# Performance work log

Measured on AMD Instinct MI355X. Metric: run time of the kernel, lower is better.

## Reference

```python
import jax, jax.numpy as jnp
import numpy as np

B, S, D, H, DFF, N_LAYERS, BLK = 4, 1024, 1024, 16, 4096, 4, 64
DH = D // H
LN_EPS = 1e-5


def setup_inputs() -> dict:
    key = jax.random.key(0)
    ks = jax.random.split(key, 13)
    s = 0.02
    L = N_LAYERS
    return {
        "x": jax.random.normal(ks[0], (B, S, D), jnp.float32),
        "in_proj_w": jax.random.normal(ks[1], (L, 3 * D, D), jnp.float32) * s,
        "in_proj_b": jnp.zeros((L, 3 * D), jnp.float32),
        "out_w": jax.random.normal(ks[2], (L, D, D), jnp.float32) * s,
        "out_b": jnp.zeros((L, D), jnp.float32),
        "ln1_w": jnp.ones((L, D), jnp.float32),
        "ln1_b": jnp.zeros((L, D), jnp.float32),
        "lin1_w": jax.random.normal(ks[3], (L, DFF, D), jnp.float32) * s,
        "lin1_b": jnp.zeros((L, DFF), jnp.float32),
        "lin2_w": jax.random.normal(ks[4], (L, D, DFF), jnp.float32) * s,
        "lin2_b": jnp.zeros((L, D), jnp.float32),
        "ln2_w": jnp.ones((L, D), jnp.float32),
        "ln2_b": jnp.zeros((L, D), jnp.float32),
    }


def _layer_norm(x, w, b):
    mu = jnp.mean(x, axis=-1, keepdims=True)
    var = jnp.mean(jnp.square(x - mu), axis=-1, keepdims=True)
    return (x - mu) * jax.lax.rsqrt(var + LN_EPS) * w + b


def _forward(x, in_proj_w, in_proj_b, out_w, out_b, ln1_w, ln1_b,
             lin1_w, lin1_b, lin2_w, lin2_b, ln2_w, ln2_b):
    # block-causal additive bias: token may attend to current and previous blocks
    blk = jnp.arange(S) // BLK
    bias = jnp.where(blk[:, None] >= blk[None, :], 0.0, -jnp.inf)  # [S,S]
    scale = 1.0 / np.sqrt(DH).astype(np.float32)

    for l in range(N_LAYERS):
        # --- self-attention (post-norm, PyTorch TransformerEncoderLayer default) ---
        qkv = x @ in_proj_w[l].T + in_proj_b[l]            # [B,S,3D]
        q, k, v = jnp.split(qkv, 3, axis=-1)
        q = q.reshape(B, S, H, DH).transpose(0, 2, 1, 3)   # [B,H,S,DH]
        k = k.reshape(B, S, H, DH).transpose(0, 2, 1, 3)
        v = v.reshape(B, S, H, DH).transpose(0, 2, 1, 3)
        scores = jnp.einsum('bhqd,bhkd->bhqk', q, k) * scale + bias
        attn = jax.nn.softmax(scores, axis=-1)
        o = jnp.einsum('bhqk,bhkd->bhqd', attn, v)
        o = o.transpose(0, 2, 1, 3).reshape(B, S, D)
        o = o @ out_w[l].T + out_b[l]
        x = _layer_norm(x + o, ln1_w[l], ln1_b[l])
        # --- feed-forward (relu) ---
        h = jax.nn.relu(x @ lin1_w[l].T + lin1_b[l]) @ lin2_w[l].T + lin2_b[l]
        x = _layer_norm(x + h, ln2_w[l], ln2_b[l])
    return x


def reference(x, in_proj_w, in_proj_b, out_w, out_b, ln1_w, ln1_b,
              lin1_w, lin1_b, lin2_w, lin2_b, ln2_w, ln2_b):
    return _forward(x, in_proj_w, in_proj_b, out_w, out_b, ln1_w, ln1_b,
                    lin1_w, lin1_b, lin2_w, lin2_b, ln2_w, ln2_b)
```

## Files before the change

### kernel.cpp

```cpp
#include <hip/hip_runtime.h>
#include <stdint.h>

typedef __bf16 bf16;
typedef __bf16 bf16x8 __attribute__((ext_vector_type(8)));
typedef __bf16 bf16x4 __attribute__((ext_vector_type(4)));
typedef float  f32x4  __attribute__((ext_vector_type(4)));

#define B_   4
#define S_   1024
#define D_   1024
#define H_   16
#define DH_  64
#define DFF_ 4096
#define NL_  4
#define M_   (B_*S_)

__device__ __forceinline__ void async_copy16(const void* g, void* l) {
  __builtin_amdgcn_global_load_lds(
      (const __attribute__((address_space(1))) char*)(uintptr_t)g,
      (__attribute__((address_space(3))) char*)(uintptr_t)l,
      16, 0, 0);
}

#define WAITV4 asm volatile("s_waitcnt vmcnt(4)" ::: "memory")
#define WAITV0 asm volatile("s_waitcnt vmcnt(0)" ::: "memory")
#define BAR()  { asm volatile("" ::: "memory"); __builtin_amdgcn_s_barrier(); \
                 asm volatile("" ::: "memory"); }

template<int RELU, int MODE, int QKV, int PH>
__global__ __launch_bounds__(512, 2) void gemm256_kernel(
    const bf16* __restrict__ A,
    const bf16* __restrict__ W,
    const float* __restrict__ bias,
    bf16*  __restrict__ Cb,
    bf16*  __restrict__ VtOut,
    int N, int Ktot, int Kc, int gx, int PN, int PM, int bpk)
{
  __shared__ __align__(16) bf16 As[2][2][256*32];
  __shared__ __align__(16) bf16 Bs[2][2][256*32];

  const int tid  = threadIdx.x;
  const int wave = tid >> 6;
  const int lane = tid & 63;
  const int wr = wave >> 2, wc = wave & 3;
  const int q4  = lane >> 4;
  const int l15 = lane & 15;

  const int Lg  = blockIdx.x;
  const int kz  = Lg / bpk;
  const int L   = Lg % bpk;
  const int xcd = L & 7;
  const int s   = L >> 3;
  const int Gn  = gx / PN;
  const int bn = ((xcd % Gn)*PN + (s % PN)) << 8;
  const int bm = ((xcd / Gn)*PM + (s / PN)) << 8;
  const int kstart = kz * Kc;

  const int r_loc = lane >> 2, c4 = lane & 3;
  const int sko = (c4 ^ ((r_loc >> 1) & 3)) << 3;
  const bf16* agp[2]; const bf16* wgp[2];
#pragma unroll
  for (int j = 0; j < 2; ++j) {
    const int rr = j*128 + wave*16 + r_loc;
    agp[j] = A + (size_t)(bm + rr)*Ktot + kstart + sko;
    wgp[j] = W + (size_t)(bn + rr)*Ktot + kstart + sko;
  }

  auto stageA = [&](int buf, int kk, int koff) {
#pragma unroll
    for (int j = 0; j < 2; ++j)
      async_copy16(agp[j] + koff + kk*32, &As[buf][kk][(j*128 + wave*16)*32]);
  };
  auto stageB = [&](int buf, int kk, int koff) {
#pragma unroll
    for (int j = 0; j < 2; ++j)
      async_copy16(wgp[j] + koff + kk*32, &Bs[buf][kk][(j*128 + wave*16)*32]);
  };

  const int ch = ((q4 ^ ((l15 >> 1) & 3)) << 3);

  f32x4 acc[8][4] = {};
  const int steps = Kc / 64;

  stageA(0, 0, 0); stageB(0, 0, 0); stageA(0, 1, 0); stageB(0, 1, 0);
  WAITV4;
  BAR();

  int koff = 64;
  for (int t = 0; t < steps; ++t) {
    const int c = t & 1;
    const bool pf = (t + 1 < steps);
    if constexpr (PH == 4) {
      bf16x8 bfr[4];
#pragma unroll
      for (int p = 0; p < 4; ++p) {
        const int kk = p >> 1, rh = p & 1;
        if (rh == 0) {
#pragma unroll
          for (int cf = 0; cf < 4; ++cf)
            bfr[cf] = *(const bf16x8*)&Bs[c][kk][(wc*64 + cf*16 + l15)*32 + ch];
        }
        bf16x8 af[4];
#pragma unroll
        for (int r4 = 0; r4 < 4; ++r4)
          af[r4] = *(const bf16x8*)&As[c][kk][(wr*128 + (rh*4 + r4)*16 + l15)*32 + ch];
        if (pf) {
          if      (p == 0) stageA(c ^ 1, 0, koff);
          else if (p == 1) stageB(c ^ 1, 0, koff);
          else if (p == 2) stageA(c ^ 1, 1, koff);
          else             stageB(c ^ 1, 1, koff);
        }
        BAR();
        __builtin_amdgcn_s_setprio(1);
#pragma unroll
        for (int r4 = 0; r4 < 4; ++r4)
#pragma unroll
          for (int cf = 0; cf < 4; ++cf)
            acc[rh*4 + r4][cf] = __builtin_amdgcn_mfma_f32_16x16x32_bf16(
                af[r4], bfr[cf], acc[rh*4 + r4][cf], 0, 0, 0);
        __builtin_amdgcn_s_setprio(0);
        if (p == 1) { if (pf) { WAITV4; } else { WAITV0; } }
        if (p == 3) { if (pf) { WAITV4; } }
        BAR();
      }
    } else {
#pragma unroll
      for (int kk = 0; kk < 2; ++kk) {
        if (pf) { stageA(c ^ 1, kk, koff); stageB(c ^ 1, kk, koff); }
        bf16x8 bfr[4];
#pragma unroll
        for (int cf = 0; cf < 4; ++cf)
          bfr[cf] = *(const bf16x8*)&Bs[c][kk][(wc*64 + cf*16 + l15)*32 + ch];
        bf16x8 af[8];
#pragma unroll
        for (int r = 0; r < 8; ++r)
          af[r] = *(const bf16x8*)&As[c][kk][(wr*128 + r*16 + l15)*32 + ch];
        BAR();
        __builtin_amdgcn_s_setprio(1);
#pragma unroll
        for (int r = 0; r < 8; ++r)
#pragma unroll
          for (int cf = 0; cf < 4; ++cf)
            acc[r][cf] = __builtin_amdgcn_mfma_f32_16x16x32_bf16(
                af[r], bfr[cf], acc[r][cf], 0, 0, 0);
        __builtin_amdgcn_s_setprio(0);
        if (kk == 0) { if (pf) { WAITV4; } else { WAITV0; } }
        else         { if (pf) { WAITV4; } }
        BAR();
      }
    }
    koff += 64;
  }

  if (QKV && bn >= 2*D_) {
#pragma unroll
    for (int r = 0; r < 8; ++r) {
      const int row0 = bm + wr*128 + r*16 + q4*4;
      const int bidx = row0 >> 10, s0 = row0 & 1023;
#pragma unroll
      for (int cf = 0; cf < 4; ++cf) {
        const int col  = bn + wc*64 + cf*16 + l15;
        const int dcol = col - 2*D_;
        const int hh = dcol >> 6, dd = dcol & 63;
        const float bv = bias[col];
        bf16x4 pk;
#pragma unroll
        for (int i = 0; i < 4; ++i) pk[i] = (bf16)(acc[r][cf][i] + bv);
        *(bf16x4*)&VtOut[((size_t)((bidx*H_ + hh)*64 + dd))*S_ + s0] = pk;
      }
    }
  } else if (MODE == 2) {
    bf16* Cpz = Cb + (size_t)kz * ((size_t)M_ * N);
#pragma unroll
    for (int r = 0; r < 8; ++r) {
      const int row0 = bm + wr*128 + r*16 + q4*4;
#pragma unroll
      for (int cf = 0; cf < 4; ++cf) {
        const int col = bn + wc*64 + cf*16 + l15;
#pragma unroll
        for (int i = 0; i < 4; ++i)
          Cpz[(size_t)(row0 + i)*N + col] = (bf16)acc[r][cf][i];
      }
    }
  } else {
#pragma unroll
    for (int r = 0; r < 8; ++r) {
      const int row0 = bm + wr*128 + r*16 + q4*4;
#pragma unroll
      for (int cf = 0; cf < 4; ++cf) {
        const int col = bn + wc*64 + cf*16 + l15;
        const float bv = bias[col];
#pragma unroll
        for (int i = 0; i < 4; ++i) {
          float v = acc[r][cf][i] + bv;
          if (RELU) v = fmaxf(v, 0.f);
          Cb[(size_t)(row0 + i)*N + col] = (bf16)v;
        }
      }
    }
  }
}

template<int RELU, int MODE, int BK>
__global__ __launch_bounds__(256) void gemm_bt_kernel(
    const bf16* __restrict__ A, const bf16* __restrict__ W,
    const float* __restrict__ bias, bf16* __restrict__ Cb,
    int N, int Ktot, int Kc, int gx, int PN, int PM, int bpk)
{
  constexpr int NI = (BK == 64) ? 4 : 2;
  __shared__ bf16 As[2][128*BK];
  __shared__ bf16 Bs[2][128*BK];

  const int tid  = threadIdx.x;
  const int wave = tid >> 6;
  const int lane = tid & 63;
  const int wr = wave >> 1, wc = wave & 1;
  const int q4  = lane >> 4;
  const int l15 = lane & 15;

  const int Lg  = blockIdx.x;
  const int kz  = Lg / bpk;
  const int L   = Lg % bpk;
  const int xcd = L & 7;
  const int s   = L >> 3;
  const int Gn  = gx / PN;
  const int bn = ((xcd % Gn)*PN + (s % PN)) << 7;
  const int bm = ((xcd / Gn)*PM + (s / PN)) << 7;
  const int kstart = kz * Kc;

  const bf16* agp[NI]; const bf16* wgp[NI];
  int ldsb[NI];
  if constexpr (BK == 64) {
    const int r_loc = lane >> 3, c8 = lane & 7;
#pragma unroll
    for (int j = 0; j < NI; ++j) {
      const int rr = wave*32 + j*8 + r_loc;
      const int ko = ((c8 ^ (rr & 7)) << 3);
      agp[j] = A + (size_t)(bm + rr)*Ktot + kstart + ko;
      wgp[j] = W + (size_t)(bn + rr)*Ktot + kstart + ko;
      ldsb[j] = (wave*32 + j*8) * 64;
    }
  } else {
    const int r_loc = lane >> 2, c4 = lane & 3;
#pragma unroll
    for (int j = 0; j < NI; ++j) {
      const int rr = wave*32 + j*16 + r_loc;
      const int ko = ((c4 ^ ((rr >> 1) & 3)) << 3);
      agp[j] = A + (size_t)(bm + rr)*Ktot + kstart + ko;
      wgp[j] = W + (size_t)(bn + rr)*Ktot + kstart + ko;
      ldsb[j] = (wave*32 + j*16) * 32;
    }
  }

  f32x4 acc[4][4] = {};
  const int steps = Kc / BK;

  auto stage = [&](int buf) {
#pragma unroll
    for (int j = 0; j < NI; ++j) {
      async_copy16(agp[j], &As[buf][ldsb[j]]);
      async_copy16(wgp[j], &Bs[buf][ldsb[j]]);
      agp[j] += BK; wgp[j] += BK;
    }
  };

  const int sl32 = (l15 >> 1) & 3;
  const int sl64 = l15 & 7;

  auto compute = [&](int buf) {
    if constexpr (BK == 64) {
#pragma unroll
      for (int kk = 0; kk < 2; ++kk) {
        const int ch = (((kk << 2) | q4) ^ sl64) << 3;
        bf16x8 af[4], bfr[4];
#pragma unroll
        for (int rf = 0; rf < 4; ++rf)
          af[rf] = *(const bf16x8*)&As[buf][(wr*64 + rf*16 + l15)*64 + ch];
#pragma unroll
        for (int cf = 0; cf < 4; ++cf)
          bfr[cf] = *(const bf16x8*)&Bs[buf][(wc*64 + cf*16 + l15)*64 + ch];
#pragma unroll
        for (int rf = 0; rf < 4; ++rf)
#pragma unroll
          for (int cf = 0; cf < 4; ++cf)
            acc[rf][cf] = __builtin_amdgcn_mfma_f32_16x16x32_bf16(
                af[rf], bfr[cf], acc[rf][cf], 0, 0, 0);
      }
    } else {
      const int ch = (q4 ^ sl32) << 3;
      bf16x8 af[4], bfr[4];
#pragma unroll
      for (int rf = 0; rf < 4; ++rf)
        af[rf] = *(const bf16x8*)&As[buf][(wr*64 + rf*16 + l15)*32 + ch];
#pragma unroll
      for (int cf = 0; cf < 4; ++cf)
        bfr[cf] = *(const bf16x8*)&Bs[buf][(wc*64 + cf*16 + l15)*32 + ch];
#pragma unroll
      for (int rf = 0; rf < 4; ++rf)
#pragma unroll
        for (int cf = 0; cf < 4; ++cf)
          acc[rf][cf] = __builtin_amdgcn_mfma_f32_16x16x32_bf16(
              af[rf], bfr[cf], acc[rf][cf], 0, 0, 0);
    }
  };

  stage(0);
  __syncthreads();
  for (int k = 0; k < steps; ++k) {
    const int cur = k & 1;
    if (k + 1 < steps) stage(cur ^ 1);
    compute(cur);
    __syncthreads();
  }

  if (MODE == 2) {
    bf16* Cpz = Cb + (size_t)kz * ((size_t)M_ * N);
#pragma unroll
    for (int r = 0; r < 4; ++r) {
      const int row0 = bm + wr*64 + r*16 + q4*4;
#pragma unroll
      for (int c = 0; c < 4; ++c) {
        const int col = bn + wc*64 + c*16 + l15;
#pragma unroll
        for (int i = 0; i < 4; ++i)
          Cpz[(size_t)(row0 + i)*N + col] = (bf16)acc[r][c][i];
      }
    }
  } else {
#pragma unroll
    for (int r = 0; r < 4; ++r) {
      const int row0 = bm + wr*64 + r*16 + q4*4;
#pragma unroll
      for (int c = 0; c < 4; ++c) {
        const int col = bn + wc*64 + c*16 + l15;
        const float bv = bias[col];
#pragma unroll
        for (int i = 0; i < 4; ++i) {
          float v = acc[r][c][i] + bv;
          if (RELU) v = fmaxf(v, 0.f);
          Cb[(size_t)(row0 + i)*N + col] = (bf16)v;
        }
      }
    }
  }
}

__global__ __launch_bounds__(256) void attn_kernel(
    const bf16* __restrict__ qkv,
    const bf16* __restrict__ vt,
    bf16* __restrict__ out)
{
  const int L    = blockIdx.x;
  const int xcd  = L & 7, slot = L >> 3;
  const int qb0  = slot & 7;
  const int bh   = xcd*8 + (slot >> 3);
  const int b    = bh >> 4, h = bh & 15;
  const int tid  = threadIdx.x;
  const int wave = tid >> 6, lane = tid & 63;
  const int q4 = lane >> 4, l15 = lane & 15;
  const int r_loc = lane >> 3, c8 = lane & 7;

  __shared__ bf16 Ks[2][64*64];
  __shared__ bf16 Vs[2][64*64];
  __shared__ bf16 Ps[4][16*64];

  const size_t RS = 3*(size_t)D_;
  const bf16* kg = qkv + (size_t)(b*S_)*RS + D_ + h*64;
  const bf16* vg = vt + (size_t)bh*64*S_;

#define STAGE_KV(KT, BUF)                                              \
  {                                                                    \
    _Pragma("unroll")                                                  \
    for (int j = 0; j < 2; ++j) {                                      \
      const int rr = wave*16 + j*8 + r_loc;                            \
      const int ko = ((c8 ^ (rr & 7)) << 3);                           \
      async_copy16(kg + (size_t)((KT)*64 + rr)*RS + ko,                \
                   &Ks[BUF][(wave*16 + j*8)*64]);                      \
      async_copy16(vg + (size_t)rr*S_ + (KT)*64 + ko,                  \
                   &Vs[BUF][(wave*16 + j*8)*64]);                      \
    }                                                                  \
  }

  for (int pass = 0; pass < 2; ++pass) {
    const int qb = pass ? (15 - qb0) : qb0;
    const bf16* qg = qkv + (size_t)(b*S_ + qb*64)*RS + h*64;

    bf16x8 qf[2];
#pragma unroll
    for (int kk = 0; kk < 2; ++kk) {
      bf16x8 t = *(const bf16x8*)(qg + (size_t)(wave*16 + l15)*RS + kk*32 + (q4 << 3));
#pragma unroll
      for (int j = 0; j < 8; ++j) t[j] = (bf16)((float)t[j] * 0.125f);
      qf[kk] = t;
    }

    f32x4 o_acc[4] = {};
    float m_i = -1e30f, l_i = 0.f;

    STAGE_KV(0, 0)
    __syncthreads();

    for (int kt = 0; kt <= qb; ++kt) {
      const int cur = kt & 1;
      if (kt < qb) {
        if (cur) STAGE_KV(kt+1, 0) else STAGE_KV(kt+1, 1)
      }

      f32x4 sc[4] = {};
#pragma unroll
      for (int kk = 0; kk < 2; ++kk) {
        const int go = ((((kk << 2) | q4)) ^ (l15 & 7)) << 3;
#pragma unroll
        for (int m = 0; m < 4; ++m) {
          bf16x8 bk = *(const bf16x8*)&Ks[cur][(m*16 + l15)*64 + go];
          sc[m] = __builtin_amdgcn_mfma_f32_16x16x32_bf16(bk, qf[kk], sc[m], 0, 0, 0);
        }
      }

      float mx0 = fmaxf(fmaxf(sc[0][0], sc[0][1]), fmaxf(sc[0][2], sc[0][3]));
      float mx1 = fmaxf(fmaxf(sc[1][0], sc[1][1]), fmaxf(sc[1][2], sc[1][3]));
      float mx2 = fmaxf(fmaxf(sc[2][0], sc[2][1]), fmaxf(sc[2][2], sc[2][3]));
      float mx3 = fmaxf(fmaxf(sc[3][0], sc[3][1]), fmaxf(sc[3][2], sc[3][3]));
      float mx  = fmaxf(fmaxf(mx0, mx1), fmaxf(mx2, mx3));
      mx = fmaxf(mx, __shfl_xor(mx, 16, 64));
      mx = fmaxf(mx, __shfl_xor(mx, 32, 64));

      if (__any(mx > m_i + 8.f)) {
        const float m_new = fmaxf(m_i, mx);
        const float alpha = __expf(m_i - m_new);
        m_i = m_new;
        l_i *= alpha;
#pragma unroll
        for (int i = 0; i < 4; ++i) {
          const float av = __shfl(alpha, (lane & 48) | ((q4 << 2) | i), 64);
#pragma unroll
          for (int c = 0; c < 4; ++c) o_acc[c][i] *= av;
        }
      }

      float rs = 0.f;
#pragma unroll
      for (int m = 0; m < 4; ++m) {
        const float p0 = __expf(sc[m][0] - m_i);
        const float p1 = __expf(sc[m][1] - m_i);
        const float p2 = __expf(sc[m][2] - m_i);
        const float p3 = __expf(sc[m][3] - m_i);
        rs += (p0 + p1) + (p2 + p3);
        bf16x4 pk;
        pk[0] = (bf16)p0; pk[1] = (bf16)p1; pk[2] = (bf16)p2; pk[3] = (bf16)p3;
        const int cx = ((m << 2) | q4) ^ (l15 & 14);
        *(bf16x4*)&Ps[wave][(l15 << 6) | (cx << 2)] = pk;
      }
      rs += __shfl_xor(rs, 16, 64);
      rs += __shfl_xor(rs, 32, 64);
      l_i += rs;

#pragma unroll
      for (int kk = 0; kk < 2; ++kk) {
        const int pcx = (((kk << 3) | (q4 << 1)) ^ (l15 & 14));
        bf16x8 ap = *(const bf16x8*)&Ps[wave][(l15 << 6) | (pcx << 2)];
        const int go = ((((kk << 2) | q4)) ^ (l15 & 7)) << 3;
#pragma unroll
        for (int c = 0; c < 4; ++c) {
          bf16x8 bv = *(const bf16x8*)&Vs[cur][(c*16 + l15)*64 + go];
          o_acc[c] = __builtin_amdgcn_mfma_f32_16x16x32_bf16(ap, bv, o_acc[c], 0, 0, 0);
        }
      }
      __syncthreads();
    }

    bf16* obase = out + ((size_t)(b*S_ + qb*64 + wave*16))*D_ + h*64;
#pragma unroll
    for (int i = 0; i < 4; ++i) {
      const float li = __shfl(l_i, (lane & 48) | ((q4 << 2) | i), 64);
      const float inv = 1.f / li;
#pragma unroll
      for (int c = 0; c < 4; ++c)
        obase[(size_t)((q4 << 2) | i)*D_ + c*16 + l15] = (bf16)(o_acc[c][i] * inv);
    }
  }
#undef STAGE_KV
}

template<int NP>
__global__ __launch_bounds__(256) void add_ln_kernel(
    const float* __restrict__ xin, const bf16* __restrict__ parts,
    const float* __restrict__ ybias,
    const float* __restrict__ w, const float* __restrict__ bta,
    float* __restrict__ xout, bf16* __restrict__ xbf,
    float* __restrict__ extra)
{
  const int row = blockIdx.x;
  const int tid = threadIdx.x;
  const size_t base = (size_t)row * D_;
  const size_t PS = (size_t)M_ * D_;
  const int i0 = tid << 2;

  float4 xi = *(const float4*)&xin[base + i0];
  float4 yb = *(const float4*)&ybias[i0];
  float v[4] = { xi.x + yb.x, xi.y + yb.y, xi.z + yb.z, xi.w + yb.w };
#pragma unroll
  for (int pz = 0; pz < NP; ++pz) {
    bf16x4 pk = *(const bf16x4*)&parts[(size_t)pz*PS + base + i0];
#pragma unroll
    for (int i = 0; i < 4; ++i) v[i] += (float)pk[i];
  }
  float sm = (v[0] + v[1]) + (v[2] + v[3]);
  float ss = (v[0]*v[0] + v[1]*v[1]) + (v[2]*v[2] + v[3]*v[3]);
#pragma unroll
  for (int off = 1; off < 64; off <<= 1) {
    sm += __shfl_xor(sm, off, 64);
    ss += __shfl_xor(ss, off, 64);
  }
  __shared__ float red[8];
  const int wave = tid >> 6, lane = tid & 63;
  if (lane == 0) { red[wave] = sm; red[4 + wave] = ss; }
  __syncthreads();
  sm = red[0] + red[1] + red[2] + red[3];
  ss = red[4] + red[5] + red[6] + red[7];
  const float mean = sm * (1.f/D_);
  const float var  = ss * (1.f/D_) - mean*mean;
  const float rstd = rsqrtf(var + 1e-5f);

  float4 wv = *(const float4*)&w[i0];
  float4 bv = *(const float4*)&bta[i0];
  float o[4];
  o[0] = (v[0] - mean)*rstd*wv.x + bv.x;
  o[1] = (v[1] - mean)*rstd*wv.y + bv.y;
  o[2] = (v[2] - mean)*rstd*wv.z + bv.z;
  o[3] = (v[3] - mean)*rstd*wv.w + bv.w;
  float4 of = { o[0], o[1], o[2], o[3] };
  *(float4*)&xout[base + i0] = of;
  bf16x4 ob;
#pragma unroll
  for (int i = 0; i < 4; ++i) ob[i] = (bf16)o[i];
  *(bf16x4*)&xbf[base + i0] = ob;
  if (extra) *(float4*)&extra[base + i0] = of;
}

__global__ __launch_bounds__(256) void conv_kernel(
    const float4* __restrict__ src, bf16x4* __restrict__ dst, int n4)
{
  int i = blockIdx.x*blockDim.x + threadIdx.x;
  const int stride = gridDim.x*blockDim.x;
  for (; i < n4; i += stride) {
    float4 f = src[i];
    bf16x4 o;
    o[0] = (bf16)f.x; o[1] = (bf16)f.y; o[2] = (bf16)f.z; o[3] = (bf16)f.w;
    dst[i] = o;
  }
}

__global__ __launch_bounds__(256) void init_x_kernel(
    const float4* __restrict__ src, float4* __restrict__ xf,
    bf16x4* __restrict__ xb, int n4)
{
  int i = blockIdx.x*blockDim.x + threadIdx.x;
  const int stride = gridDim.x*blockDim.x;
  for (; i < n4; i += stride) {
    float4 f = src[i];
    xf[i] = f;
    bf16x4 o;
    o[0] = (bf16)f.x; o[1] = (bf16)f.y; o[2] = (bf16)f.z; o[3] = (bf16)f.w;
    xb[i] = o;
  }
}

extern "C" void kernel_launch(void* const* d_in, const int* in_sizes, int n_in,
                              void* d_out, int out_size, void* d_ws, size_t ws_size,
                              hipStream_t stream) {
  const float* x    = (const float*)d_in[0];
  const float* inw  = (const float*)d_in[1];
  const float* inb  = (const float*)d_in[2];
  const float* outw = (const float*)d_in[3];
  const float* outb = (const float*)d_in[4];
  const float* ln1w = (const float*)d_in[5];
  const float* ln1b = (const float*)d_in[6];
  const float* l1w  = (const float*)d_in[7];
  const float* l1b  = (const float*)d_in[8];
  const float* l2w  = (const float*)d_in[9];
  const float* l2b  = (const float*)d_in[10];
  const float* ln2w = (const float*)d_in[11];
  const float* ln2b = (const float*)d_in[12];

  char* ws = (char*)d_ws;
  size_t off = 0;
  auto take = [&](size_t bytes) {
    char* p = ws + off;
    off = (off + bytes + 255) & ~(size_t)255;
    return p;
  };
  bf16*  w_in_bf  = (bf16*) take((size_t)NL_*3*D_*D_*2);
  bf16*  w_out_bf = (bf16*) take((size_t)NL_*D_*D_*2);
  bf16*  w_l1_bf  = (bf16*) take((size_t)NL_*DFF_*D_*2);
  bf16*  w_l2_bf  = (bf16*) take((size_t)NL_*D_*DFF_*2);
  float* x_f      = (float*)take((size_t)M_*D_*4);
  bf16*  x_b      = (bf16*) take((size_t)M_*D_*2);
  bf16*  qkv_b    = (bf16*) take((size_t)M_*3*D_*2);
  bf16*  vt_b     = (bf16*) take((size_t)B_*H_*DH_*S_*2);
  bf16*  at_b     = (bf16*) take((size_t)M_*D_*2);
  bf16*  h_b      = (bf16*) take((size_t)M_*DFF_*2);
  bf16*  parts    = (bf16*) take((size_t)4*M_*D_*2);
  (void)ws_size; (void)in_sizes; (void)n_in;

  auto conv = [&](const float* s, bf16* d, size_t n) {
    int n4 = (int)(n >> 2);
    int grid = (n4 + 255) / 256; if (grid > 4096) grid = 4096;
    conv_kernel<<<grid, 256, 0, stream>>>((const float4*)s, (bf16x4*)d, n4);
  };
  conv(inw,  w_in_bf,  (size_t)NL_*3*D_*D_);
  conv(outw, w_out_bf, (size_t)NL_*D_*D_);
  conv(l1w,  w_l1_bf,  (size_t)NL_*DFF_*D_);
  conv(l2w,  w_l2_bf,  (size_t)NL_*D_*DFF_);
  init_x_kernel<<<4096, 256, 0, stream>>>((const float4*)x, (float4*)x_f,
                                          (bf16x4*)x_b, (int)((size_t)M_*D_ >> 2));

  for (int l = 0; l < NL_; ++l) {
    gemm256_kernel<0,1,1,2><<<192, 512, 0, stream>>>(
        x_b, w_in_bf + (size_t)l*3*D_*D_, inb + (size_t)l*3*D_,
        qkv_b, vt_b, 3*D_, D_, D_, 12, 3, 8, 192);
    attn_kernel<<<512, 256, 0, stream>>>(qkv_b, vt_b, at_b);
    gemm_bt_kernel<0,2,64><<<512, 256, 0, stream>>>(
        at_b, w_out_bf + (size_t)l*D_*D_, nullptr,
        parts, D_, D_, D_/2, 8, 4, 8, 256);
    add_ln_kernel<2><<<M_, 256, 0, stream>>>(
        x_f, parts, outb + (size_t)l*D_,
        ln1w + (size_t)l*D_, ln1b + (size_t)l*D_, x_f, x_b, nullptr);
    gemm256_kernel<1,1,0,4><<<256, 512, 0, stream>>>(
        x_b, w_l1_bf + (size_t)l*DFF_*D_, l1b + (size_t)l*DFF_,
        h_b, nullptr, DFF_, D_, D_, 16, 4, 8, 256);
    gemm256_kernel<0,2,0,4><<<256, 512, 0, stream>>>(
        h_b, w_l2_bf + (size_t)l*D_*DFF_, nullptr,
        parts, nullptr, D_, DFF_, DFF_/4, 4, 1, 8, 64);
    add_ln_kernel<4><<<M_, 256, 0, stream>>>(
        x_f, parts, l2b + (size_t)l*D_,
        ln2w + (size_t)l*D_, ln2b + (size_t)l*D_, x_f, x_b,
        (l == NL_-1) ? (float*)d_out : nullptr);
  }
}
```

Baseline: 971.1 us.

## Use explicit vmcnt waits with barriers in GEMM/attention pipelines; merge weight conversions

Replaces __syncthreads around the double-buffered async global-to-LDS staging in the GEMM and attention kernels with explicit s_waitcnt vmcnt plus raw s_barrier. The next tile's loads can then stay in flight while the current tile is computed, instead of being drained by a full fence. It also merges the four weight-conversion launches into one kernel. The risk is that the vmcnt counts must match exactly the number of outstanding loads per stage, or reads will race with copies still landing in LDS.

```diff
diff --git a/kernel.cpp b/kernel.cpp
--- a/kernel.cpp
+++ b/kernel.cpp
@@ -22,6 +22,7 @@
       16, 0, 0);
 }
 
+#define WAITV8 asm volatile("s_waitcnt vmcnt(8)" ::: "memory")
 #define WAITV4 asm volatile("s_waitcnt vmcnt(4)" ::: "memory")
 #define WAITV0 asm volatile("s_waitcnt vmcnt(0)" ::: "memory")
 #define BAR()  { asm volatile("" ::: "memory"); __builtin_amdgcn_s_barrier(); \
@@ -305,12 +306,14 @@
   };
 
   stage(0);
-  __syncthreads();
   for (int k = 0; k < steps; ++k) {
     const int cur = k & 1;
-    if (k + 1 < steps) stage(cur ^ 1);
+    const bool pf = (k + 1 < steps);
+    if (pf) stage(cur ^ 1);
+    if (pf) { WAITV8; } else { WAITV0; }
+    BAR();
     compute(cur);
-    __syncthreads();
+    BAR();
   }
 
   if (MODE == 2) {
@@ -398,13 +401,16 @@
     float m_i = -1e30f, l_i = 0.f;
 
     STAGE_KV(0, 0)
-    __syncthreads();
 
     for (int kt = 0; kt <= qb; ++kt) {
       const int cur = kt & 1;
       if (kt < qb) {
         if (cur) STAGE_KV(kt+1, 0) else STAGE_KV(kt+1, 1)
-      }
+        WAITV4;
+      } else {
+        WAITV0;
+      }
+      BAR();
 
       f32x4 sc[4] = {};
 #pragma unroll
@@ -466,7 +472,7 @@
           o_acc[c] = __builtin_amdgcn_mfma_f32_16x16x32_bf16(ap, bv, o_acc[c], 0, 0, 0);
         }
       }
-      __syncthreads();
+      BAR();
     }
 
     bf16* obase = out + ((size_t)(b*S_ + qb*64 + wave*16))*D_ + h*64;
@@ -538,17 +544,26 @@
   if (extra) *(float4*)&extra[base + i0] = of;
 }
 
-__global__ __launch_bounds__(256) void conv_kernel(
-    const float4* __restrict__ src, bf16x4* __restrict__ dst, int n4)
+__global__ __launch_bounds__(256) void conv_all_kernel(
+    const float4* __restrict__ s0, bf16x4* __restrict__ d0, int n0,
+    const float4* __restrict__ s1, bf16x4* __restrict__ d1, int n1,
+    const float4* __restrict__ s2, bf16x4* __restrict__ d2, int n2,
+    const float4* __restrict__ s3, bf16x4* __restrict__ d3, int n3)
 {
-  int i = blockIdx.x*blockDim.x + threadIdx.x;
+  const int t0 = blockIdx.x*blockDim.x + threadIdx.x;
   const int stride = gridDim.x*blockDim.x;
-  for (; i < n4; i += stride) {
-    float4 f = src[i];
-    bf16x4 o;
-    o[0] = (bf16)f.x; o[1] = (bf16)f.y; o[2] = (bf16)f.z; o[3] = (bf16)f.w;
-    dst[i] = o;
-  }
+#define CSEG(S, DPTR, N)                                     \
+  for (int i = t0; i < (N); i += stride) {                   \
+    float4 f = (S)[i];                                       \
+    bf16x4 o;                                                \
+    o[0]=(bf16)f.x; o[1]=(bf16)f.y; o[2]=(bf16)f.z; o[3]=(bf16)f.w; \
+    (DPTR)[i] = o;                                           \
+  }
+  CSEG(s0, d0, n0)
+  CSEG(s1, d1, n1)
+  CSEG(s2, d2, n2)
+  CSEG(s3, d3, n3)
+#undef CSEG
 }
 
 __global__ __launch_bounds__(256) void init_x_kernel(
@@ -603,15 +618,11 @@
   bf16*  parts    = (bf16*) take((size_t)4*M_*D_*2);
   (void)ws_size; (void)in_sizes; (void)n_in;
 
-  auto conv = [&](const float* s, bf16* d, size_t n) {
-    int n4 = (int)(n >> 2);
-    int grid = (n4 + 255) / 256; if (grid > 4096) grid = 4096;
-    conv_kernel<<<grid, 256, 0, stream>>>((const float4*)s, (bf16x4*)d, n4);
-  };
-  conv(inw,  w_in_bf,  (size_t)NL_*3*D_*D_);
-  conv(outw, w_out_bf, (size_t)NL_*D_*D_);
-  conv(l1w,  w_l1_bf,  (size_t)NL_*DFF_*D_);
-  conv(l2w,  w_l2_bf,  (size_t)NL_*D_*DFF_);
+  conv_all_kernel<<<4096, 256, 0, stream>>>(
+      (const float4*)inw,  (bf16x4*)w_in_bf,  (int)(((size_t)NL_*3*D_*D_) >> 2),
+      (const float4*)outw, (bf16x4*)w_out_bf, (int)(((size_t)NL_*D_*D_) >> 2),
+      (const float4*)l1w,  (bf16x4*)w_l1_bf,  (int)(((size_t)NL_*DFF_*D_) >> 2),
+      (const float4*)l2w,  (bf16x4*)w_l2_bf,  (int)(((size_t)NL_*D_*DFF_) >> 2));
   init_x_kernel<<<4096, 256, 0, stream>>>((const float4*)x, (float4*)x_f,
                                           (bf16x4*)x_b, (int)((size_t)M_*D_ >> 2));
 
```

Measured after the change: 974.7 us. About the same (+0.4%).

## Overlap next-tile prefetch with compute via partial vmcnt waits; unroll conversion kernels

Applied to the files above, without the earlier changes.

Replaces the full __syncthreads after staging in the GEMM and attention loops with explicit s_waitcnt vmcnt(N) waits plus raw barriers. The current tile's async global-to-LDS loads are waited on while the next tile's loads stay in flight, so prefetch overlaps with MFMA compute. The weight and input conversion kernels are unrolled by four with a smaller fixed grid to put more loads in flight per thread. The partial-wait correctness depends on exact per-thread counts of outstanding vector memory ops matching 8 and 4, and a miscount could cause data races.

```diff
diff --git a/kernel.cpp b/kernel.cpp
--- a/kernel.cpp
+++ b/kernel.cpp
@@ -22,6 +22,7 @@
       16, 0, 0);
 }
 
+#define WAITV8 asm volatile("s_waitcnt vmcnt(8)" ::: "memory")
 #define WAITV4 asm volatile("s_waitcnt vmcnt(4)" ::: "memory")
 #define WAITV0 asm volatile("s_waitcnt vmcnt(0)" ::: "memory")
 #define BAR()  { asm volatile("" ::: "memory"); __builtin_amdgcn_s_barrier(); \
@@ -305,12 +306,14 @@
   };
 
   stage(0);
-  __syncthreads();
   for (int k = 0; k < steps; ++k) {
     const int cur = k & 1;
-    if (k + 1 < steps) stage(cur ^ 1);
+    const bool pf = (k + 1 < steps);
+    if (pf) stage(cur ^ 1);
+    if (pf) { WAITV8; } else { WAITV0; }
+    BAR();
     compute(cur);
-    __syncthreads();
+    BAR();
   }
 
   if (MODE == 2) {
@@ -398,13 +401,16 @@
     float m_i = -1e30f, l_i = 0.f;
 
     STAGE_KV(0, 0)
-    __syncthreads();
 
     for (int kt = 0; kt <= qb; ++kt) {
       const int cur = kt & 1;
       if (kt < qb) {
         if (cur) STAGE_KV(kt+1, 0) else STAGE_KV(kt+1, 1)
-      }
+        WAITV4;
+      } else {
+        WAITV0;
+      }
+      BAR();
 
       f32x4 sc[4] = {};
 #pragma unroll
@@ -466,7 +472,7 @@
           o_acc[c] = __builtin_amdgcn_mfma_f32_16x16x32_bf16(ap, bv, o_acc[c], 0, 0, 0);
         }
       }
-      __syncthreads();
+      BAR();
     }
 
     bf16* obase = out + ((size_t)(b*S_ + qb*64 + wave*16))*D_ + h*64;
@@ -538,31 +544,51 @@
   if (extra) *(float4*)&extra[base + i0] = of;
 }
 
+__device__ __forceinline__ bf16x4 cvt4(float4 f) {
+  bf16x4 o;
+  o[0] = (bf16)f.x; o[1] = (bf16)f.y; o[2] = (bf16)f.z; o[3] = (bf16)f.w;
+  return o;
+}
+
 __global__ __launch_bounds__(256) void conv_kernel(
     const float4* __restrict__ src, bf16x4* __restrict__ dst, int n4)
 {
+  const int T = gridDim.x*blockDim.x;
   int i = blockIdx.x*blockDim.x + threadIdx.x;
-  const int stride = gridDim.x*blockDim.x;
-  for (; i < n4; i += stride) {
-    float4 f = src[i];
-    bf16x4 o;
-    o[0] = (bf16)f.x; o[1] = (bf16)f.y; o[2] = (bf16)f.z; o[3] = (bf16)f.w;
-    dst[i] = o;
-  }
+  for (; i + 3*T < n4; i += 4*T) {
+    float4 f0 = src[i];
+    float4 f1 = src[i +   T];
+    float4 f2 = src[i + 2*T];
+    float4 f3 = src[i + 3*T];
+    dst[i]       = cvt4(f0);
+    dst[i +   T] = cvt4(f1);
+    dst[i + 2*T] = cvt4(f2);
+    dst[i + 3*T] = cvt4(f3);
+  }
+  for (; i < n4; i += T) dst[i] = cvt4(src[i]);
 }
 
 __global__ __launch_bounds__(256) void init_x_kernel(
     const float4* __restrict__ src, float4* __restrict__ xf,
     bf16x4* __restrict__ xb, int n4)
 {
+  const int T = gridDim.x*blockDim.x;
   int i = blockIdx.x*blockDim.x + threadIdx.x;
-  const int stride = gridDim.x*blockDim.x;
-  for (; i < n4; i += stride) {
+  for (; i + 3*T < n4; i += 4*T) {
+    float4 f0 = src[i];
+    float4 f1 = src[i +   T];
+    float4 f2 = src[i + 2*T];
+    float4 f3 = src[i + 3*T];
+    xf[i] = f0; xf[i + T] = f1; xf[i + 2*T] = f2; xf[i + 3*T] = f3;
+    xb[i]       = cvt4(f0);
+    xb[i +   T] = cvt4(f1);
+    xb[i + 2*T] = cvt4(f2);
+    xb[i + 3*T] = cvt4(f3);
+  }
+  for (; i < n4; i += T) {
     float4 f = src[i];
     xf[i] = f;
-    bf16x4 o;
-    o[0] = (bf16)f.x; o[1] = (bf16)f.y; o[2] = (bf16)f.z; o[3] = (bf16)f.w;
-    xb[i] = o;
+    xb[i] = cvt4(f);
   }
 }
 
@@ -604,15 +630,14 @@
   (void)ws_size; (void)in_sizes; (void)n_in;
 
   auto conv = [&](const float* s, bf16* d, size_t n) {
-    int n4 = (int)(n >> 2);
-    int grid = (n4 + 255) / 256; if (grid > 4096) grid = 4096;
-    conv_kernel<<<grid, 256, 0, stream>>>((const float4*)s, (bf16x4*)d, n4);
+    conv_kernel<<<1024, 256, 0, stream>>>((const float4*)s, (bf16x4*)d,
+                                          (int)(n >> 2));
   };
   conv(inw,  w_in_bf,  (size_t)NL_*3*D_*D_);
   conv(outw, w_out_bf, (size_t)NL_*D_*D_);
   conv(l1w,  w_l1_bf,  (size_t)NL_*DFF_*D_);
   conv(l2w,  w_l2_bf,  (size_t)NL_*D_*DFF_);
-  init_x_kernel<<<4096, 256, 0, stream>>>((const float4*)x, (float4*)x_f,
+  init_x_kernel<<<1024, 256, 0, stream>>>((const float4*)x, (float4*)x_f,
                                           (bf16x4*)x_b, (int)((size_t)M_*D_ >> 2));
 
   for (int l = 0; l < NL_; ++l) {
```

Result: no change. 978.7 us (+0.8%).
